# Performance work log

Hardware: AMD Instinct MI355X
Metric: run time of the kernel (lower is better)

Reference implementation:

```python
import jax, jax.numpy as jnp
import numpy as np

NUM_TILES = 512
N_POINTS = 512
D_IN = 256
D_OUT = 256
CHANNELS = 1024


def setup_inputs() -> dict:
    key = jax.random.key(0)
    k1, k2, k3 = jax.random.split(key, 3)
    x = jax.random.normal(k1, (NUM_TILES, N_POINTS, D_IN), dtype=jnp.float32)
    indices = jax.random.randint(k2, (NUM_TILES,), 0, CHANNELS, dtype=jnp.int64)
    # kaiming-uniform-like init for the per-channel weight tiles
    bound = float(np.sqrt(6.0 / D_IN))
    weight = jax.random.uniform(k3, (CHANNELS, D_IN, D_OUT), dtype=jnp.float32,
                                minval=-bound, maxval=bound)
    bias = jnp.zeros((1, 1, D_OUT), dtype=jnp.float32)
    return {"x": x, "indices": indices, "weight": weight, "bias": bias}


def reference(x, indices, weight, bias):
    # gather per-tile weights [T, D_in, D_out], then batched matmul
    w = weight[indices]  # [T, D_in, D_out]
    # [T, P, D_in] @ [T, D_in, D_out] -> [T, P, D_out]
    out = jnp.einsum('tpi,tio->tpo', x, w) + bias[0]
    return out
```

## Files before the change

### kernel.cpp

```cpp
#include <hip/hip_runtime.h>
#include <hip/hip_bf16.h>

typedef __attribute__((ext_vector_type(8))) short bf16x8;
typedef __attribute__((ext_vector_type(4))) short bf16x4;
typedef __attribute__((ext_vector_type(4))) float f32x4;

constexpr int NT   = 512;
constexpr int NP   = 512;
constexpr int DIN  = 256;
constexpr int DOUT = 256;

__device__ __forceinline__ short f2bf(float f) {
  __hip_bfloat16 h = __float2bfloat16(f);
  return __builtin_bit_cast(short, h);
}

__device__ __forceinline__ int wsw(int n, int k) {
  return n * DIN + (k ^ (((n >> 1) & 7) << 3));
}

__device__ __forceinline__ int xsw(int m, int k) {
  return m * 64 + (k ^ ((m & 7) << 3));
}

__global__ __launch_bounds__(512, 2) void adaptive_linear_v3(
    const float* __restrict__ x,
    const int*   __restrict__ idx,
    const float* __restrict__ w,
    const float* __restrict__ bias,
    float*       __restrict__ out)
{
  __shared__ short Ws[DOUT * DIN];
  __shared__ short Xs[128 * 64];

  const int tid = threadIdx.x;
  const int t   = blockIdx.x;

  const int c = idx[t];
  const float* xb = x   + (size_t)t * NP * DIN;
  const float* wb = w   + (size_t)c * DIN * DOUT;
  float*       ob = out + (size_t)t * NP * DOUT;

  const int wl = tid & 63;
  const int wv = tid >> 6;
  const int xrow = tid >> 2;
  const int xo   = (tid & 3) * 4;

  f32x4 wr[8];
  f32x4 xr[4];

  auto load_w = [&](int ss) {
    const float* ws = wb + (size_t)(ss * 64 + wv * 8) * DOUT + wl * 4;
    #pragma unroll
    for (int q = 0; q < 8; ++q)
      wr[q] = *reinterpret_cast<const f32x4*>(ws + (size_t)q * DOUT);
  };
  auto write_w = [&](int ss) {
    #pragma unroll
    for (int h = 0; h < 2; ++h) {
      const int k0 = ss * 64 + wv * 8 + h * 4;
      #pragma unroll
      for (int j = 0; j < 4; ++j) {
        bf16x4 v = { f2bf(wr[h*4+0][j]), f2bf(wr[h*4+1][j]),
                     f2bf(wr[h*4+2][j]), f2bf(wr[h*4+3][j]) };
        *reinterpret_cast<bf16x4*>(&Ws[wsw(wl * 4 + j, k0)]) = v;
      }
    }
  };
  auto load_x = [&](int s) {
    const int c4 = s >> 2, ks = s & 3;
    const float* xs = xb + (size_t)(c4 * 128 + xrow) * DIN + ks * 64 + xo;
    #pragma unroll
    for (int i = 0; i < 4; ++i)
      xr[i] = *reinterpret_cast<const f32x4*>(xs + i * 16);
  };
  auto write_x = [&]() {
    #pragma unroll
    for (int i = 0; i < 4; ++i) {
      const int k0 = i * 16 + xo;
      bf16x4 v = { f2bf(xr[i][0]), f2bf(xr[i][1]),
                   f2bf(xr[i][2]), f2bf(xr[i][3]) };
      *reinterpret_cast<bf16x4*>(&Xs[xsw(xrow, k0)]) = v;
    }
  };

  const int l    = tid & 63;
  const int wid  = tid >> 6;
  const int wm   = wid >> 2;
  const int wn   = wid & 3;
  const int lrow = l & 15;
  const int lk   = l >> 4;

  float bv[4];
  #pragma unroll
  for (int fn = 0; fn < 4; ++fn)
    bv[fn] = bias[wn * 64 + fn * 16 + lrow];

  load_w(0);
  load_x(0);
  write_w(0);
  write_x();
  __syncthreads();

  f32x4 acc[4][4] = {};

  for (int c4 = 0; c4 < 4; ++c4) {
    #pragma unroll
    for (int ks = 0; ks < 4; ++ks) {
      const int s = c4 * 4 + ks;

      if (s < 15) load_x(s + 1);
      if (s < 3)  load_w(s + 1);

      #pragma unroll
      for (int kc = 0; kc < 2; ++kc) {
        const int kb = kc * 32 + lk * 8;
        bf16x8 a[4], b[4];
        #pragma unroll
        for (int fm = 0; fm < 4; ++fm)
          a[fm] = *reinterpret_cast<const bf16x8*>(
              &Xs[xsw(wm * 64 + fm * 16 + lrow, kb)]);
        #pragma unroll
        for (int fn = 0; fn < 4; ++fn)
          b[fn] = *reinterpret_cast<const bf16x8*>(
              &Ws[wsw(wn * 64 + fn * 16 + lrow, ks * 64 + kb)]);
        #pragma unroll
        for (int fm = 0; fm < 4; ++fm)
          #pragma unroll
          for (int fn = 0; fn < 4; ++fn)
            acc[fm][fn] = __builtin_amdgcn_mfma_f32_16x16x32_bf16(
                a[fm], b[fn], acc[fm][fn], 0, 0, 0);
      }

      if (ks == 3) {
        #pragma unroll
        for (int fm = 0; fm < 4; ++fm) {
          const int r0w = c4 * 128 + wm * 64 + fm * 16 + lk * 4;
          #pragma unroll
          for (int fn = 0; fn < 4; ++fn) {
            const int col = wn * 64 + fn * 16 + lrow;
            float* op = ob + (size_t)r0w * DOUT + col;
            #pragma unroll
            for (int rr = 0; rr < 4; ++rr)
              __builtin_nontemporal_store(acc[fm][fn][rr] + bv[fn],
                                          op + (size_t)rr * DOUT);
          }
        }
        #pragma unroll
        for (int fm = 0; fm < 4; ++fm)
          #pragma unroll
          for (int fn = 0; fn < 4; ++fn)
            acc[fm][fn] = f32x4{0.f, 0.f, 0.f, 0.f};
      }

      __syncthreads();
      if (s < 15) write_x();
      if (s < 3)  write_w(s + 1);
      __syncthreads();
    }
  }
}

extern "C" void kernel_launch(void* const* d_in, const int* in_sizes, int n_in,
                              void* d_out, int out_size, void* d_ws, size_t ws_size,
                              hipStream_t stream) {
  const float* x    = (const float*)d_in[0];
  const int*   idx  = (const int*)d_in[1];
  const float* w    = (const float*)d_in[2];
  const float* bias = (const float*)d_in[3];
  float* out = (float*)d_out;

  adaptive_linear_v3<<<NT, 512, 0, stream>>>(x, idx, w, bias, out);
}
```

Baseline: 149.1 us.

## Double-buffer X tile in LDS and drop to one barrier per step

Splits the X shared tile into two buffers and adds a second register stage, so each step loads X two steps ahead and writes the next buffer before its MFMA work. The weight tile's remaining slices are also written during compute. This removes one of the two barriers per K-step and overlaps LDS writes with matrix math. It also changes the weight LDS swizzle to reduce bank conflicts and swaps nontemporal output stores for plain stores. In exchange it raises LDS use to the full 160KB and adds register pressure.

```diff
diff --git a/kernel.cpp b/kernel.cpp
--- a/kernel.cpp
+++ b/kernel.cpp
@@ -16,14 +16,14 @@
 }
 
 __device__ __forceinline__ int wsw(int n, int k) {
-  return n * DIN + (k ^ (((n >> 1) & 7) << 3));
+  return n * DIN + (k ^ (((n ^ (n >> 2)) & 7) << 3));
 }
 
 __device__ __forceinline__ int xsw(int m, int k) {
   return m * 64 + (k ^ ((m & 7) << 3));
 }
 
-__global__ __launch_bounds__(512, 2) void adaptive_linear_v3(
+__global__ __launch_bounds__(512, 2) void adaptive_linear_v4(
     const float* __restrict__ x,
     const int*   __restrict__ idx,
     const float* __restrict__ w,
@@ -31,7 +31,7 @@
     float*       __restrict__ out)
 {
   __shared__ short Ws[DOUT * DIN];
-  __shared__ short Xs[128 * 64];
+  __shared__ short Xs[2][128 * 64];
 
   const int tid = threadIdx.x;
   const int t   = blockIdx.x;
@@ -47,7 +47,7 @@
   const int xo   = (tid & 3) * 4;
 
   f32x4 wr[8];
-  f32x4 xr[4];
+  f32x4 xr[2][4];
 
   auto load_w = [&](int ss) {
     const float* ws = wb + (size_t)(ss * 64 + wv * 8) * DOUT + wl * 4;
@@ -67,20 +67,20 @@
       }
     }
   };
-  auto load_x = [&](int s) {
-    const int c4 = s >> 2, ks = s & 3;
-    const float* xs = xb + (size_t)(c4 * 128 + xrow) * DIN + ks * 64 + xo;
+  auto load_x = [&](int s, int p) {
+    const int cc = s >> 2, kk = s & 3;
+    const float* xs = xb + (size_t)(cc * 128 + xrow) * DIN + kk * 64 + xo;
     #pragma unroll
     for (int i = 0; i < 4; ++i)
-      xr[i] = *reinterpret_cast<const f32x4*>(xs + i * 16);
+      xr[p][i] = *reinterpret_cast<const f32x4*>(xs + i * 16);
   };
-  auto write_x = [&]() {
+  auto write_x = [&](int p, int b) {
     #pragma unroll
     for (int i = 0; i < 4; ++i) {
       const int k0 = i * 16 + xo;
-      bf16x4 v = { f2bf(xr[i][0]), f2bf(xr[i][1]),
-                   f2bf(xr[i][2]), f2bf(xr[i][3]) };
-      *reinterpret_cast<bf16x4*>(&Xs[xsw(xrow, k0)]) = v;
+      bf16x4 v = { f2bf(xr[p][i][0]), f2bf(xr[p][i][1]),
+                   f2bf(xr[p][i][2]), f2bf(xr[p][i][3]) };
+      *reinterpret_cast<bf16x4*>(&Xs[b][xsw(xrow, k0)]) = v;
     }
   };
 
@@ -97,9 +97,11 @@
     bv[fn] = bias[wn * 64 + fn * 16 + lrow];
 
   load_w(0);
-  load_x(0);
+  load_x(0, 0);
   write_w(0);
-  write_x();
+  write_x(0, 0);
+  load_w(1);
+  load_x(1, 1);
   __syncthreads();
 
   f32x4 acc[4][4] = {};
@@ -109,8 +111,14 @@
     for (int ks = 0; ks < 4; ++ks) {
       const int s = c4 * 4 + ks;
 
-      if (s < 15) load_x(s + 1);
-      if (s < 3)  load_w(s + 1);
+      if (s < 14) load_x(s + 2, ks & 1);
+
+      if (s < 15) write_x((ks + 1) & 1, (ks + 1) & 1);
+
+      if (c4 == 0 && ks < 3) {
+        write_w(ks + 1);
+        if (ks < 2) load_w(ks + 2);
+      }
 
       #pragma unroll
       for (int kc = 0; kc < 2; ++kc) {
@@ -119,7 +127,7 @@
         #pragma unroll
         for (int fm = 0; fm < 4; ++fm)
           a[fm] = *reinterpret_cast<const bf16x8*>(
-              &Xs[xsw(wm * 64 + fm * 16 + lrow, kb)]);
+              &Xs[ks & 1][xsw(wm * 64 + fm * 16 + lrow, kb)]);
         #pragma unroll
         for (int fn = 0; fn < 4; ++fn)
           b[fn] = *reinterpret_cast<const bf16x8*>(
@@ -142,8 +150,7 @@
             float* op = ob + (size_t)r0w * DOUT + col;
             #pragma unroll
             for (int rr = 0; rr < 4; ++rr)
-              __builtin_nontemporal_store(acc[fm][fn][rr] + bv[fn],
-                                          op + (size_t)rr * DOUT);
+              op[(size_t)rr * DOUT] = acc[fm][fn][rr] + bv[fn];
           }
         }
         #pragma unroll
@@ -153,10 +160,7 @@
             acc[fm][fn] = f32x4{0.f, 0.f, 0.f, 0.f};
       }
 
-      __syncthreads();
-      if (s < 15) write_x();
-      if (s < 3)  write_w(s + 1);
-      __syncthreads();
+      if (s < 15) __syncthreads();
     }
   }
 }
@@ -170,5 +174,5 @@
   const float* bias = (const float*)d_in[3];
   float* out = (float*)d_out;
 
-  adaptive_linear_v3<<<NT, 512, 0, stream>>>(x, idx, w, bias, out);
+  adaptive_linear_v4<<<NT, 512, 0, stream>>>(x, idx, w, bias, out);
 }
```

Result: faster. 136.3 us (-8.6%).

## Restructure to load full weight tile upfront and stream x in 64-row chunks

Applied to the files above, without the earlier changes.

Loads and converts the whole 256x256 weight tile into shared memory before the main loop, then processes x in eight 64-row chunks with full K=256 per chunk, prefetching the next chunk into registers. This halves the barrier count per chunk, shrinks accumulators to 2x4 fragments, changes the W swizzle, and replaces __syncthreads with a custom lgkmcnt wait plus s_barrier. Output stores become regular stores instead of nontemporal. Risks include a longer serial prologue, less MFMA work per barrier, and shared memory of roughly 160KB per block, which may limit occupancy below the requested two blocks.

```diff
diff --git a/kernel.cpp b/kernel.cpp
--- a/kernel.cpp
+++ b/kernel.cpp
@@ -9,21 +9,28 @@
 constexpr int NP   = 512;
 constexpr int DIN  = 256;
 constexpr int DOUT = 256;
+constexpr int CHM  = 64;
 
 __device__ __forceinline__ short f2bf(float f) {
   __hip_bfloat16 h = __float2bfloat16(f);
   return __builtin_bit_cast(short, h);
 }
 
+__device__ __forceinline__ void wg_barrier() {
+  asm volatile("s_waitcnt lgkmcnt(0)" ::: "memory");
+  __builtin_amdgcn_s_barrier();
+  __builtin_amdgcn_sched_barrier(0);
+}
+
 __device__ __forceinline__ int wsw(int n, int k) {
-  return n * DIN + (k ^ (((n >> 1) & 7) << 3));
+  return n * DIN + (k ^ (((n ^ (n >> 2)) & 7) << 3));
 }
 
 __device__ __forceinline__ int xsw(int m, int k) {
-  return m * 64 + (k ^ ((m & 7) << 3));
+  return m * DIN + (k ^ ((m & 7) << 3));
 }
 
-__global__ __launch_bounds__(512, 2) void adaptive_linear_v3(
+__global__ __launch_bounds__(512, 2) void adaptive_linear_v7(
     const float* __restrict__ x,
     const int*   __restrict__ idx,
     const float* __restrict__ w,
@@ -31,7 +38,7 @@
     float*       __restrict__ out)
 {
   __shared__ short Ws[DOUT * DIN];
-  __shared__ short Xs[128 * 64];
+  __shared__ short Xs[CHM * DIN];
 
   const int tid = threadIdx.x;
   const int t   = blockIdx.x;
@@ -43,11 +50,7 @@
 
   const int wl = tid & 63;
   const int wv = tid >> 6;
-  const int xrow = tid >> 2;
-  const int xo   = (tid & 3) * 4;
-
   f32x4 wr[8];
-  f32x4 xr[4];
 
   auto load_w = [&](int ss) {
     const float* ws = wb + (size_t)(ss * 64 + wv * 8) * DOUT + wl * 4;
@@ -67,20 +70,22 @@
       }
     }
   };
-  auto load_x = [&](int s) {
-    const int c4 = s >> 2, ks = s & 3;
-    const float* xs = xb + (size_t)(c4 * 128 + xrow) * DIN + ks * 64 + xo;
+
+  f32x4 xr[8];
+  auto load_x = [&](int ch) {
+    const float* base = xb + (size_t)ch * CHM * DIN;
     #pragma unroll
-    for (int i = 0; i < 4; ++i)
-      xr[i] = *reinterpret_cast<const f32x4*>(xs + i * 16);
+    for (int i = 0; i < 8; ++i)
+      xr[i] = *reinterpret_cast<const f32x4*>(base + i * 2048 + tid * 4);
   };
   auto write_x = [&]() {
+    const int m0 = tid >> 6;
+    const int k  = (tid & 63) * 4;
     #pragma unroll
-    for (int i = 0; i < 4; ++i) {
-      const int k0 = i * 16 + xo;
+    for (int i = 0; i < 8; ++i) {
       bf16x4 v = { f2bf(xr[i][0]), f2bf(xr[i][1]),
                    f2bf(xr[i][2]), f2bf(xr[i][3]) };
-      *reinterpret_cast<bf16x4*>(&Xs[xsw(xrow, k0)]) = v;
+      *reinterpret_cast<bf16x4*>(&Xs[xsw(m0 + i * 8, k)]) = v;
     }
   };
 
@@ -96,67 +101,56 @@
   for (int fn = 0; fn < 4; ++fn)
     bv[fn] = bias[wn * 64 + fn * 16 + lrow];
 
+  load_x(0);
   load_w(0);
-  load_x(0);
   write_w(0);
+  load_w(1); write_w(1);
+  load_w(2); write_w(2);
+  load_w(3); write_w(3);
   write_x();
-  __syncthreads();
+  wg_barrier();
 
-  f32x4 acc[4][4] = {};
+  for (int ch = 0; ch < 8; ++ch) {
+    if (ch < 7) load_x(ch + 1);
 
-  for (int c4 = 0; c4 < 4; ++c4) {
+    f32x4 acc[2][4] = {};
     #pragma unroll
-    for (int ks = 0; ks < 4; ++ks) {
-      const int s = c4 * 4 + ks;
-
-      if (s < 15) load_x(s + 1);
-      if (s < 3)  load_w(s + 1);
-
+    for (int ks = 0; ks < 8; ++ks) {
+      const int kb = ks * 32 + lk * 8;
+      bf16x8 a[2], b[4];
       #pragma unroll
-      for (int kc = 0; kc < 2; ++kc) {
-        const int kb = kc * 32 + lk * 8;
-        bf16x8 a[4], b[4];
-        #pragma unroll
-        for (int fm = 0; fm < 4; ++fm)
-          a[fm] = *reinterpret_cast<const bf16x8*>(
-              &Xs[xsw(wm * 64 + fm * 16 + lrow, kb)]);
+      for (int fm = 0; fm < 2; ++fm)
+        a[fm] = *reinterpret_cast<const bf16x8*>(
+            &Xs[xsw(wm * 32 + fm * 16 + lrow, kb)]);
+      #pragma unroll
+      for (int fn = 0; fn < 4; ++fn)
+        b[fn] = *reinterpret_cast<const bf16x8*>(
+            &Ws[wsw(wn * 64 + fn * 16 + lrow, kb)]);
+      #pragma unroll
+      for (int fm = 0; fm < 2; ++fm)
         #pragma unroll
         for (int fn = 0; fn < 4; ++fn)
-          b[fn] = *reinterpret_cast<const bf16x8*>(
-              &Ws[wsw(wn * 64 + fn * 16 + lrow, ks * 64 + kb)]);
+          acc[fm][fn] = __builtin_amdgcn_mfma_f32_16x16x32_bf16(
+              a[fm], b[fn], acc[fm][fn], 0, 0, 0);
+    }
+
+    #pragma unroll
+    for (int fm = 0; fm < 2; ++fm) {
+      const int r0w = ch * CHM + wm * 32 + fm * 16 + lk * 4;
+      #pragma unroll
+      for (int fn = 0; fn < 4; ++fn) {
+        const int col = wn * 64 + fn * 16 + lrow;
+        float* op = ob + (size_t)r0w * DOUT + col;
         #pragma unroll
-        for (int fm = 0; fm < 4; ++fm)
-          #pragma unroll
-          for (int fn = 0; fn < 4; ++fn)
-            acc[fm][fn] = __builtin_amdgcn_mfma_f32_16x16x32_bf16(
-                a[fm], b[fn], acc[fm][fn], 0, 0, 0);
+        for (int rr = 0; rr < 4; ++rr)
+          op[(size_t)rr * DOUT] = acc[fm][fn][rr] + bv[fn];
       }
+    }
 
-      if (ks == 3) {
-        #pragma unroll
-        for (int fm = 0; fm < 4; ++fm) {
-          const int r0w = c4 * 128 + wm * 64 + fm * 16 + lk * 4;
-          #pragma unroll
-          for (int fn = 0; fn < 4; ++fn) {
-            const int col = wn * 64 + fn * 16 + lrow;
-            float* op = ob + (size_t)r0w * DOUT + col;
-            #pragma unroll
-            for (int rr = 0; rr < 4; ++rr)
-              __builtin_nontemporal_store(acc[fm][fn][rr] + bv[fn],
-                                          op + (size_t)rr * DOUT);
-          }
-        }
-        #pragma unroll
-        for (int fm = 0; fm < 4; ++fm)
-          #pragma unroll
-          for (int fn = 0; fn < 4; ++fn)
-            acc[fm][fn] = f32x4{0.f, 0.f, 0.f, 0.f};
-      }
-
-      __syncthreads();
-      if (s < 15) write_x();
-      if (s < 3)  write_w(s + 1);
-      __syncthreads();
+    if (ch < 7) {
+      wg_barrier();
+      write_x();
+      wg_barrier();
     }
   }
 }
@@ -170,5 +164,5 @@
   const float* bias = (const float*)d_in[3];
   float* out = (float*)d_out;
 
-  adaptive_linear_v3<<<NT, 512, 0, stream>>>(x, idx, w, bias, out);
+  adaptive_linear_v7<<<NT, 512, 0, stream>>>(x, idx, w, bias, out);
 }
```

After: 135.0 us. 1.1x faster.
